# Performance work log

Hardware: AMD Instinct MI355X
Metric: run time of the kernel (lower is better)

The kernel has to match this reference:

```python
import jax, jax.numpy as jnp
import numpy as np

B, Cin, H, W = 8, 256, 32, 32
KS, NH, K = 32, 8, 5          # key_size == value_size, num_heads, kernel_size
STRIDE, PAD = 1, 2
Cout = KS * 3 * NH            # 768
EPS = 1e-5


def setup_inputs() -> dict:
    key = jax.random.key(0)
    k0, k1, k2 = jax.random.split(key, 3)
    return {
        "x": jax.random.normal(k0, (B, Cin, H, W), jnp.float32),
        "conv_w": jax.random.normal(k1, (Cout, Cin), jnp.float32) / np.sqrt(Cin).astype(np.float32),
        "conv_b": jax.random.normal(k2, (Cout,), jnp.float32) * 0.02,
        "gn_w": jnp.ones((Cout,), jnp.float32),
        "gn_b": jnp.zeros((Cout,), jnp.float32),
    }


def reference(x, conv_w, conv_b, gn_w, gn_b):
    Bb = x.shape[0]
    OH = (H + 2 * PAD - K) // STRIDE + 1
    OW = (W + 2 * PAD - K) // STRIDE + 1

    # 1x1 conv: (B, Cout, H, W)
    attn = jnp.einsum('bchw,oc->bohw', x, conv_w) + conv_b[None, :, None, None]

    # unfold / Tile2d -> (B, KH, KW, Cout, OH, OW)
    ap = jnp.pad(attn, ((0, 0), (0, 0), (PAD, PAD), (PAD, PAD)))
    rows = []
    for kh in range(K):
        cols = [ap[:, :, kh:kh + OH * STRIDE:STRIDE, kw:kw + OW * STRIDE:STRIDE]
                for kw in range(K)]
        rows.append(jnp.stack(cols, axis=1))          # (B, KW, C, OH, OW)
    tiles = jnp.stack(rows, axis=1)                   # (B, KH, KW, C, OH, OW)

    # GroupNorm over (group_channels, OH, OW) per (b, kh, kw) sample.
    # groups = 3*NH, group size = KS (each head's key/query/value chunk).
    G = 3 * NH
    t = tiles.reshape(Bb, K, K, G, KS, OH, OW)
    mean = t.mean(axis=(4, 5, 6), keepdims=True)
    var = t.var(axis=(4, 5, 6), keepdims=True)        # biased, like torch GroupNorm
    t = (t - mean) * jax.lax.rsqrt(var + EPS)
    t = t.reshape(Bb, K, K, Cout, OH, OW)
    t = t * gn_w[None, None, None, :, None, None] + gn_b[None, None, None, :, None, None]

    # (B, OH, OW, NH, 3*KS, KH*KW)
    t = t.transpose(0, 4, 5, 3, 1, 2).reshape(Bb, OH, OW, NH, 3 * KS, K * K)
    keyt = t[..., :KS, :]            # (B, OH, OW, NH, KS, KK)
    qt = t[..., KS:2 * KS, :]
    vt = t[..., 2 * KS:, :]          # (B, OH, OW, NH, VS, KK)

    q = qt.mean(axis=-1)             # mean query over the window: (B, OH, OW, NH, KS)
    sal = jnp.einsum('bijnk,bijnkp->bijnp', q, keyt) / np.float32(np.sqrt(KS))
    mask = jax.nn.softmax(sal, axis=-1)               # (B, OH, OW, NH, KK)
    out = jnp.einsum('bijnvp,bijnp->bijnv', vt, mask)  # (B, OH, OW, NH, VS)

    out = out.transpose(0, 3, 4, 1, 2).reshape(Bb, NH * KS, OH, OW)
    return out
```

## Files before the change

kernel.cpp:

```cpp
#include <hip/hip_runtime.h>
#include <hip/hip_bf16.h>

#define B_    8
#define CIN   256
#define COUT  768
#define G_    24
#define PW    40
#define PLANE 1440
#define EPS_  1e-5f

typedef float f32x4 __attribute__((ext_vector_type(4)));
typedef short s16x8 __attribute__((ext_vector_type(8)));
typedef unsigned short ushort_t;
typedef unsigned short u16x4 __attribute__((ext_vector_type(4)));
typedef unsigned long long ull_t;

#define LDS_FENCE() do { asm volatile("" ::: "memory"); \
                         __builtin_amdgcn_s_waitcnt(0xC07F); \
                         asm volatile("" ::: "memory"); } while (0)

static __device__ __forceinline__ ushort_t f2bf(float f) {
    union { float f; unsigned u; } a; a.f = f;
    const unsigned u = a.u;
    const unsigned r = u + 0x7FFFu + ((u >> 16) & 1u);
    return (ushort_t)(r >> 16);
}
static __device__ __forceinline__ float bf2f(ushort_t h) {
    union { unsigned u; float f; } a; a.u = ((unsigned)h) << 16; return a.f;
}
static __device__ __forceinline__ void st4(float* dst, u16x4 v) {
    *(f32x4*)dst = f32x4{ bf2f(v[0]), bf2f(v[1]), bf2f(v[2]), bf2f(v[3]) };
}
static __device__ __forceinline__ unsigned pk2(float lo, float hi) {
    return (unsigned)f2bf(lo) | ((unsigned)f2bf(hi) << 16);
}

__launch_bounds__(256)
__global__ void prep(const float* __restrict__ x, const float* __restrict__ wsrc,
                     ushort_t* __restrict__ xT, ushort_t* __restrict__ wbf) {
    const int bid = blockIdx.x;
    const int t = threadIdx.x;
    if (bid < 512) {
        const int nt = bid & 15, kt = (bid >> 4) & 3, b = bid >> 6;
        const int n0 = nt * 64, k0 = kt * 64;
        __shared__ float Ts[64][65];
        const int kr = t >> 2, c4 = t & 3;
        const float* src = x + (size_t)b * (CIN * 1024) + (size_t)(k0 + kr) * 1024 + n0 + c4 * 16;
        const float4 v0 = *(const float4*)(src + 0);
        const float4 v1 = *(const float4*)(src + 4);
        const float4 v2 = *(const float4*)(src + 8);
        const float4 v3 = *(const float4*)(src + 12);
        float* d = &Ts[kr][c4 * 16];
        *(float4*)(d + 0) = v0; *(float4*)(d + 4) = v1;
        *(float4*)(d + 8) = v2; *(float4*)(d + 12) = v3;
        __syncthreads();
        const int nr = t >> 2, k4 = t & 3;
        unsigned pk[8];
        #pragma unroll
        for (int i = 0; i < 8; ++i)
            pk[i] = pk2(Ts[k4 * 16 + 2 * i][nr], Ts[k4 * 16 + 2 * i + 1][nr]);
        ushort_t* dst = xT + (size_t)b * (1024 * 256) + (size_t)(n0 + nr) * 256 + k0 + k4 * 16;
        *(uint4*)(dst + 0) = uint4{ pk[0], pk[1], pk[2], pk[3] };
        *(uint4*)(dst + 8) = uint4{ pk[4], pk[5], pk[6], pk[7] };
    } else {
        const int wid = bid - 512;
        const size_t idx = (size_t)wid * 2048 + (size_t)t * 8;
        const float4 u0 = *(const float4*)(wsrc + idx);
        const float4 u1 = *(const float4*)(wsrc + idx + 4);
        uint4 o;
        o.x = pk2(u0.x, u0.y); o.y = pk2(u0.z, u0.w);
        o.z = pk2(u1.x, u1.y); o.w = pk2(u1.z, u1.w);
        *(uint4*)(wbf + idx) = o;
    }
}

__launch_bounds__(256)
__global__ void conv_gemm(const ushort_t* __restrict__ wbf, const ushort_t* __restrict__ xT,
                          const float* __restrict__ bias, ushort_t* __restrict__ attn,
                          float* __restrict__ rowAgg) {
    const int t = threadIdx.x;
    const int wv = t >> 6, lane = t & 63;
    const int q = lane >> 4, l15 = lane & 15;
    const int m0 = blockIdx.y * 64;
    const int mw = wv * 16;
    const int n_t = blockIdx.x * 64;
    const int b = n_t >> 10, nl0 = n_t & 1023;
    const int y0 = nl0 >> 5;

    __shared__ ushort_t Bs[64][264];
    ushort_t (*Ct)[2][44] = (ushort_t (*)[2][44])(&Bs[0][0]);
    float (*red)[11]      = (float (*)[11])((char*)(&Bs[0][0]) + 64 * 2 * 44 * 2);

    {
        const ushort_t* src = xT + (size_t)b * (1024 * 256) + (size_t)nl0 * 256;
        #pragma unroll
        for (int i = 0; i < 8; ++i) {
            const int id = i * 256 + t;
            const int row = id >> 5, seg = id & 31;
            *(s16x8*)&Bs[row][seg * 8] = *(const s16x8*)(src + row * 256 + seg * 8);
        }
    }
    __syncthreads();

    const ushort_t* aPf = wbf + (size_t)(m0 + mw + l15) * 256 + q * 8;

    f32x4 acc[4] = {{0,0,0,0},{0,0,0,0},{0,0,0,0},{0,0,0,0}};
    #pragma unroll
    for (int k0 = 0; k0 < 256; k0 += 32) {
        const s16x8 a = *(const s16x8*)(aPf + k0);
        const int kk = k0 + q * 8;
        const s16x8 b0 = *(const s16x8*)&Bs[l15 +  0][kk];
        const s16x8 b1 = *(const s16x8*)&Bs[l15 + 16][kk];
        const s16x8 b2 = *(const s16x8*)&Bs[l15 + 32][kk];
        const s16x8 b3 = *(const s16x8*)&Bs[l15 + 48][kk];
        acc[0] = __builtin_amdgcn_mfma_f32_16x16x32_bf16(a, b0, acc[0], 0, 0, 0);
        acc[1] = __builtin_amdgcn_mfma_f32_16x16x32_bf16(a, b1, acc[1], 0, 0, 0);
        acc[2] = __builtin_amdgcn_mfma_f32_16x16x32_bf16(a, b2, acc[2], 0, 0, 0);
        acc[3] = __builtin_amdgcn_mfma_f32_16x16x32_bf16(a, b3, acc[3], 0, 0, 0);
    }
    __syncthreads();

    float bb[4];
    #pragma unroll
    for (int r = 0; r < 4; ++r) bb[r] = bias[m0 + mw + q * 4 + r];
    #pragma unroll
    for (int j = 0; j < 4; ++j) {
        const int yy = j >> 1, xx = (j & 1) * 16 + l15;
        #pragma unroll
        for (int r = 0; r < 4; ++r)
            Ct[mw + q * 4 + r][yy][2 + xx] = f2bf(acc[j][r] + bb[r]);
    }
    #pragma unroll
    for (int it = 0; it < 2; ++it) {
        const int id = it * 256 + t;
        const int m = id >> 3, yy = (id >> 2) & 1, pos = id & 3;
        const int us = (pos == 0) ? 0 : (32 + 2 * pos);
        *(unsigned*)&Ct[m][yy][us] = 0u;
    }
    __syncthreads();

    ushort_t* pb = attn + ((size_t)(b * COUT + m0)) * PLANE;
    #pragma unroll
    for (int it = 0; it < 5; ++it) {
        const int id = it * 256 + t;
        const int m = id / 20, rem = id % 20, yy = rem / 10, s = rem % 10;
        const ull_t v = *(const ull_t*)&Ct[m][yy][s * 4];
        *(ull_t*)(pb + (size_t)m * PLANE + (y0 + yy + 2) * PW + s * 4) = v;
    }
    if (y0 == 0 || y0 == 30) {
        const int rowA = (y0 == 0) ? 0 : 34;
        #pragma unroll
        for (int it = 0; it < 5; ++it) {
            const int id = it * 256 + t;
            const int m = id / 20, rem = id % 20, yy = rem / 10, s = rem % 10;
            *(ull_t*)(pb + (size_t)m * PLANE + (rowA + yy) * PW + s * 4) = 0ull;
        }
    }

    if (t < 128) {
        const int gi = t >> 6, yy = (t >> 5) & 1, c = t & 31;
        const int m = gi * 32 + c;
        float lin = 0.f, sq = 0.f, e0 = 0.f, e1 = 0.f, e30 = 0.f, e31 = 0.f;
        #pragma unroll
        for (int u = 0; u < 9; ++u) {
            const ull_t vv = *(const ull_t*)&Ct[m][yy][u * 4];
            const unsigned lo = (unsigned)vv, hi = (unsigned)(vv >> 32);
            union { unsigned u; float f; } f0, f1, f2, f3;
            f0.u = lo << 16; f1.u = lo & 0xffff0000u;
            f2.u = hi << 16; f3.u = hi & 0xffff0000u;
            lin += (f0.f + f1.f) + (f2.f + f3.f);
            sq  += (f0.f * f0.f + f1.f * f1.f) + (f2.f * f2.f + f3.f * f3.f);
            if (u == 0) { e0 = f2.f; e1 = f3.f; }
            if (u == 8) { e30 = f0.f; e31 = f1.f; }
        }
        red[t][0] = lin; red[t][1] = sq;
        red[t][2] = e0;  red[t][3] = e0 * e0;
        red[t][4] = e1;  red[t][5] = e1 * e1;
        red[t][6] = e30; red[t][7] = e30 * e30;
        red[t][8] = e31; red[t][9] = e31 * e31;
    }
    __syncthreads();
    if (t < 40) {
        const int s = t % 10, gy = t / 10;
        const int gi = gy >> 1, yy = gy & 1;
        float sum = 0.f;
        #pragma unroll
        for (int c = 0; c < 32; ++c) sum += red[gi * 64 + yy * 32 + c][s];
        const int g = blockIdx.y * 2 + gi;
        rowAgg[(((size_t)b * G_ + g) * 32 + (y0 + yy)) * 10 + s] = sum;
    }
}

__launch_bounds__(128)
__global__ void local_attn(const ushort_t* __restrict__ attn,
                           const float* __restrict__ rowAgg,
                           const float* __restrict__ gn_w, const float* __restrict__ gn_b,
                           float* __restrict__ out) {
    const int wid = blockIdx.x;
    const int b = wid >> 7;
    const int n = (wid >> 4) & 7;
    const int i0 = (wid & 15) * 2;
    const int t = threadIdx.x;
    const int h = t >> 6;
    const int lane = t & 63;
    const int r = lane >> 5;
    const int j = lane & 31;

    __shared__ float KB[2][2][240];
    __shared__ float QB[2][2][240];
    __shared__ float ex[128][27];
    __shared__ float rpL[96][5], rp2L[96][5];
    __shared__ float s_m[75], s_r[75];
    __shared__ float s_rq[25], s_mq[25], s_rk[25], s_ck[25], s_rv[25], s_cv[25];
    __shared__ float s_gw[96], s_gb[96];

    if (t < 96) { s_gw[t] = gn_w[n * 96 + t]; s_gb[t] = gn_b[n * 96 + t]; }

    const float* rab = rowAgg + (size_t)((b * G_ + n * 3) * 32) * 10;
    if (t < 96) {
        const float* a = rab + (size_t)t * 10;
        const float S = a[0], Sq = a[1];
        const float e0 = a[2], q0 = a[3], e1 = a[4], q1 = a[5];
        const float e30 = a[6], q30 = a[7], e31 = a[8], q31 = a[9];
        rpL[t][0] = S - e30 - e31; rpL[t][1] = S - e31; rpL[t][2] = S;
        rpL[t][3] = S - e0;        rpL[t][4] = S - e0 - e1;
        rp2L[t][0] = Sq - q30 - q31; rp2L[t][1] = Sq - q31; rp2L[t][2] = Sq;
        rp2L[t][3] = Sq - q0;        rp2L[t][4] = Sq - q0 - q1;
    }
    __syncthreads();

    if (t < 75) {
        const int gi = t / 25, p = t % 25;
        const int kw = p % 5, kh = p / 5;
        const int rb = gi * 32;
        float cs = 0.f, cs2 = 0.f;
        #pragma unroll
        for (int yy = 0; yy < 32; ++yy) { cs += rpL[rb + yy][kw]; cs2 += rp2L[rb + yy][kw]; }
        if (kh == 0)      { cs -= rpL[rb + 30][kw] + rpL[rb + 31][kw]; cs2 -= rp2L[rb + 30][kw] + rp2L[rb + 31][kw]; }
        else if (kh == 1) { cs -= rpL[rb + 31][kw];                    cs2 -= rp2L[rb + 31][kw]; }
        else if (kh == 3) { cs -= rpL[rb + 0][kw];                     cs2 -= rp2L[rb + 0][kw]; }
        else if (kh == 4) { cs -= rpL[rb + 0][kw] + rpL[rb + 1][kw];   cs2 -= rp2L[rb + 0][kw] + rp2L[rb + 1][kw]; }
        const float inv_n = 1.f / 32768.f;
        const float mean = cs * inv_n;
        const float var  = cs2 * inv_n - mean * mean;
        s_m[t] = mean;
        s_r[t] = rsqrtf(var + EPS_);
    }
    __syncthreads();

    if (t < 25) {
        const float mK = s_m[t],      rK = s_r[t];
        const float mQ = s_m[25 + t], rQ = s_r[25 + t];
        const float mV = s_m[50 + t], rV = s_r[50 + t];
        s_rk[t] = rK; s_ck[t] = mK * rK;
        s_rq[t] = rQ; s_mq[t] = mQ * rQ;
        s_rv[t] = rV; s_cv[t] = mV * rV;
    }
    __syncthreads();

    float rq[25]; float cQ = 0.f;
    #pragma unroll
    for (int p = 0; p < 25; ++p) { rq[p] = s_rq[p]; cQ += s_mq[p]; }

    const ushort_t* regB = attn + (size_t)(b * COUT + n * 96) * PLANE + i0 * PW;
    const bool stg = (lane < 60);
    const int eo = lane * 4;
    const int base = r * PW + j;

    const ushort_t* baseK = regB + (size_t)(h * 16) * PLANE;
    const ushort_t* baseQ = regB + (size_t)(32 + h * 16) * PLANE;
    const ushort_t* baseV = regB + (size_t)(64 + h * 16) * PLANE;

    u16x4 nK{0,0,0,0}, nQ{0,0,0,0}, fK{0,0,0,0}, fQ{0,0,0,0};
    if (stg) {
        const u16x4 c0K = *(const u16x4*)(baseK + eo);
        const u16x4 c0Q = *(const u16x4*)(baseQ + eo);
        st4(&KB[h][0][eo], c0K);
        st4(&QB[h][0][eo], c0Q);
        nK = *(const u16x4*)(baseK + (size_t)PLANE + eo);
        nQ = *(const u16x4*)(baseQ + (size_t)PLANE + eo);
        fK = *(const u16x4*)(baseK + 2 * (size_t)PLANE + eo);
        fQ = *(const u16x4*)(baseQ + 2 * (size_t)PLANE + eo);
    }
    LDS_FENCE();

    float sal[25];
    #pragma unroll
    for (int p = 0; p < 25; ++p) sal[p] = 0.f;
    float sumQ2 = 0.f, sumQB = 0.f;

    for (int cc = 0; cc < 16; ++cc) {
        const int buf = cc & 1;
        if (stg && cc < 15) {
            st4(&KB[h][buf ^ 1][eo], nK);
            st4(&QB[h][buf ^ 1][eo], nQ);
            nK = fK; nQ = fQ;
            if (cc < 13) {
                fK = *(const u16x4*)(baseK + (size_t)(cc + 3) * PLANE + eo);
                fQ = *(const u16x4*)(baseQ + (size_t)(cc + 3) * PLANE + eo);
            } else if (cc == 13) {
                fK = *(const u16x4*)(baseV + eo);
                fQ = *(const u16x4*)(baseV + (size_t)PLANE + eo);
            }
        }
        const int ch = h * 16 + cc;
        const float* qb = &QB[h][buf][base];
        const float* kb = &KB[h][buf][base];
        float qa0 = 0.f, qa1 = 0.f, qa2 = 0.f, qa3 = 0.f, qa4 = 0.f;
        #pragma unroll
        for (int kw = 0; kw < 5; ++kw) {
            qa0 += rq[0 * 5 + kw] * qb[0 * PW + kw];
            qa1 += rq[1 * 5 + kw] * qb[1 * PW + kw];
            qa2 += rq[2 * 5 + kw] * qb[2 * PW + kw];
            qa3 += rq[3 * 5 + kw] * qb[3 * PW + kw];
            qa4 += rq[4 * 5 + kw] * qb[4 * PW + kw];
        }
        const float qa = (qa0 + qa1) + (qa2 + qa3) + qa4;
        const float qk  = s_gw[32 + ch] * ((qa - cQ) * 0.04f) + s_gb[32 + ch];
        const float qk2 = qk * s_gw[ch];
        sumQ2 += qk2; sumQB += qk * s_gb[ch];
        #pragma unroll
        for (int kh = 0; kh < 5; ++kh)
            #pragma unroll
            for (int kw = 0; kw < 5; ++kw)
                sal[kh * 5 + kw] += qk2 * kb[kh * PW + kw];
        LDS_FENCE();
    }

    #pragma unroll
    for (int p = 0; p < 25; ++p) ex[t][p] = sal[p];
    ex[t][25] = sumQ2; ex[t][26] = sumQB;
    if (stg) st4(&KB[h][0][eo], nK);
    __syncthreads();
    const int par = t ^ 64;
    #pragma unroll
    for (int p = 0; p < 25; ++p) sal[p] += ex[par][p];
    sumQ2 += ex[par][25]; sumQB += ex[par][26];

    u16x4 vA = nQ, vB{0,0,0,0};
    if (stg) vB = *(const u16x4*)(baseV + 2 * (size_t)PLANE + eo);

    #pragma unroll
    for (int p = 0; p < 25; ++p) sal[p] = s_rk[p] * sal[p] - s_ck[p] * sumQ2 + sumQB;

    const float scale = 0.17677669529663687f;
    float mmax = -3.4e38f;
    #pragma unroll
    for (int p = 0; p < 25; ++p) { sal[p] *= scale; mmax = fmaxf(mmax, sal[p]); }
    float ssum = 0.f;
    #pragma unroll
    for (int p = 0; p < 25; ++p) { sal[p] = __expf(sal[p] - mmax); ssum += sal[p]; }
    const float rs = 1.f / ssum;
    float cV2 = 0.f;
    #pragma unroll
    for (int p = 0; p < 25; ++p) {
        const float m = sal[p] * rs;
        sal[p] = m * s_rv[p];
        cV2 += m * s_cv[p];
    }
    LDS_FENCE();

    for (int cc = 0; cc < 16; ++cc) {
        const int buf = cc & 1;
        if (stg && cc < 15) {
            st4(&KB[h][buf ^ 1][eo], vA);
            vA = vB;
            if (cc < 13) vB = *(const u16x4*)(baseV + (size_t)(cc + 3) * PLANE + eo);
        }
        const int v = h * 16 + cc;
        const float* vb = &KB[h][buf][base];
        float a0 = 0.f, a1 = 0.f, a2 = 0.f, a3 = 0.f, a4 = 0.f;
        #pragma unroll
        for (int kw = 0; kw < 5; ++kw) {
            a0 += sal[0 * 5 + kw] * vb[0 * PW + kw];
            a1 += sal[1 * 5 + kw] * vb[1 * PW + kw];
            a2 += sal[2 * 5 + kw] * vb[2 * PW + kw];
            a3 += sal[3 * 5 + kw] * vb[3 * PW + kw];
            a4 += sal[4 * 5 + kw] * vb[4 * PW + kw];
        }
        const float acc = (a0 + a1) + (a2 + a3) + a4;
        out[((size_t)(b * 256 + n * 32 + v) * 32 + (i0 + r)) * 32 + j] =
            s_gw[64 + v] * acc + (s_gb[64 + v] - s_gw[64 + v] * cV2);
        LDS_FENCE();
    }
}

extern "C" void kernel_launch(void* const* d_in, const int* in_sizes, int n_in,
                              void* d_out, int out_size, void* d_ws, size_t ws_size,
                              hipStream_t stream) {
    const float* x      = (const float*)d_in[0];
    const float* conv_w = (const float*)d_in[1];
    const float* conv_b = (const float*)d_in[2];
    const float* gn_w   = (const float*)d_in[3];
    const float* gn_b   = (const float*)d_in[4];
    float* out = (float*)d_out;

    ushort_t* attn    = (ushort_t*)d_ws;
    float*    rowAgg  = (float*)(attn + 8847360);
    ushort_t* xT      = (ushort_t*)(rowAgg + 61440);
    ushort_t* wbf     = xT + 2097152;

    prep<<<608, 256, 0, stream>>>(x, conv_w, xT, wbf);
    conv_gemm<<<dim3(128, 12), 256, 0, stream>>>(wbf, xT, conv_b, attn, rowAgg);
    local_attn<<<1024, 128, 0, stream>>>(attn, rowAgg, gn_w, gn_b, out);
}
```

Measured before the change: 110.2 us.

## Deepen register prefetch pipeline and swizzle block order across XCDs

Global loads of K/Q/V planes are now prefetched four channels ahead through a rotating set of eight register vectors instead of two ahead. The V prefetch is chained from the tail of the K/Q loop so loads for the value phase are in flight early. Both channel loops are fully unrolled. Block indices are remapped so each group of blocks sharing a batch lands on the same XCD, which should improve L2 reuse. The costs are higher register pressure, larger code size, and fiddly index bookkeeping in the rotating buffers.

```diff
diff --git a/kernel.cpp b/kernel.cpp
--- a/kernel.cpp
+++ b/kernel.cpp
@@ -196,7 +196,8 @@
                            const float* __restrict__ rowAgg,
                            const float* __restrict__ gn_w, const float* __restrict__ gn_b,
                            float* __restrict__ out) {
-    const int wid = blockIdx.x;
+    const int bx = blockIdx.x;
+    const int wid = (bx & 7) * 128 + (bx >> 3);
     const int b = wid >> 7;
     const int n = (wid >> 4) & 7;
     const int i0 = (wid & 15) * 2;
@@ -271,16 +272,21 @@
     const ushort_t* baseQ = regB + (size_t)(32 + h * 16) * PLANE;
     const ushort_t* baseV = regB + (size_t)(64 + h * 16) * PLANE;
 
-    u16x4 nK{0,0,0,0}, nQ{0,0,0,0}, fK{0,0,0,0}, fQ{0,0,0,0};
+    u16x4 k1{0,0,0,0}, k2{0,0,0,0}, k3{0,0,0,0}, k4{0,0,0,0};
+    u16x4 q1{0,0,0,0}, q2{0,0,0,0}, q3{0,0,0,0}, q4{0,0,0,0};
     if (stg) {
         const u16x4 c0K = *(const u16x4*)(baseK + eo);
         const u16x4 c0Q = *(const u16x4*)(baseQ + eo);
         st4(&KB[h][0][eo], c0K);
         st4(&QB[h][0][eo], c0Q);
-        nK = *(const u16x4*)(baseK + (size_t)PLANE + eo);
-        nQ = *(const u16x4*)(baseQ + (size_t)PLANE + eo);
-        fK = *(const u16x4*)(baseK + 2 * (size_t)PLANE + eo);
-        fQ = *(const u16x4*)(baseQ + 2 * (size_t)PLANE + eo);
+        k1 = *(const u16x4*)(baseK + 1 * (size_t)PLANE + eo);
+        q1 = *(const u16x4*)(baseQ + 1 * (size_t)PLANE + eo);
+        k2 = *(const u16x4*)(baseK + 2 * (size_t)PLANE + eo);
+        q2 = *(const u16x4*)(baseQ + 2 * (size_t)PLANE + eo);
+        k3 = *(const u16x4*)(baseK + 3 * (size_t)PLANE + eo);
+        q3 = *(const u16x4*)(baseQ + 3 * (size_t)PLANE + eo);
+        k4 = *(const u16x4*)(baseK + 4 * (size_t)PLANE + eo);
+        q4 = *(const u16x4*)(baseQ + 4 * (size_t)PLANE + eo);
     }
     LDS_FENCE();
 
@@ -289,18 +295,20 @@
     for (int p = 0; p < 25; ++p) sal[p] = 0.f;
     float sumQ2 = 0.f, sumQB = 0.f;
 
+    #pragma unroll
     for (int cc = 0; cc < 16; ++cc) {
         const int buf = cc & 1;
         if (stg && cc < 15) {
-            st4(&KB[h][buf ^ 1][eo], nK);
-            st4(&QB[h][buf ^ 1][eo], nQ);
-            nK = fK; nQ = fQ;
-            if (cc < 13) {
-                fK = *(const u16x4*)(baseK + (size_t)(cc + 3) * PLANE + eo);
-                fQ = *(const u16x4*)(baseQ + (size_t)(cc + 3) * PLANE + eo);
-            } else if (cc == 13) {
-                fK = *(const u16x4*)(baseV + eo);
-                fQ = *(const u16x4*)(baseV + (size_t)PLANE + eo);
+            st4(&KB[h][buf ^ 1][eo], k1);
+            st4(&QB[h][buf ^ 1][eo], q1);
+            k1 = k2; k2 = k3; k3 = k4;
+            q1 = q2; q2 = q3; q3 = q4;
+            if (cc < 11) {
+                k4 = *(const u16x4*)(baseK + (size_t)(cc + 5) * PLANE + eo);
+                q4 = *(const u16x4*)(baseQ + (size_t)(cc + 5) * PLANE + eo);
+            } else {
+                k4 = *(const u16x4*)(baseV + (size_t)(cc - 11) * PLANE + eo);
+                q4 = *(const u16x4*)(baseV + (size_t)(cc - 7) * PLANE + eo);
             }
         }
         const int ch = h * 16 + cc;
@@ -330,15 +338,12 @@
     #pragma unroll
     for (int p = 0; p < 25; ++p) ex[t][p] = sal[p];
     ex[t][25] = sumQ2; ex[t][26] = sumQB;
-    if (stg) st4(&KB[h][0][eo], nK);
+    if (stg) st4(&KB[h][0][eo], k1);
     __syncthreads();
     const int par = t ^ 64;
     #pragma unroll
     for (int p = 0; p < 25; ++p) sal[p] += ex[par][p];
     sumQ2 += ex[par][25]; sumQB += ex[par][26];
-
-    u16x4 vA = nQ, vB{0,0,0,0};
-    if (stg) vB = *(const u16x4*)(baseV + 2 * (size_t)PLANE + eo);
 
     #pragma unroll
     for (int p = 0; p < 25; ++p) sal[p] = s_rk[p] * sal[p] - s_ck[p] * sumQ2 + sumQB;
@@ -360,12 +365,14 @@
     }
     LDS_FENCE();
 
+    #pragma unroll
     for (int cc = 0; cc < 16; ++cc) {
         const int buf = cc & 1;
         if (stg && cc < 15) {
-            st4(&KB[h][buf ^ 1][eo], vA);
-            vA = vB;
-            if (cc < 13) vB = *(const u16x4*)(baseV + (size_t)(cc + 3) * PLANE + eo);
+            st4(&KB[h][buf ^ 1][eo], k2);
+            k2 = k3; k3 = k4; k4 = q1; q1 = q2; q2 = q3; q3 = q4;
+            if (cc < 8)
+                q4 = *(const u16x4*)(baseV + (size_t)(cc + 8) * PLANE + eo);
         }
         const int v = h * 16 + cc;
         const float* vb = &KB[h][buf][base];
```

Measured after the change: 202.6 us. 1.84x slower.

## Double conv GEMM M-tile to reuse shared B tile; remap local_attn block order

Applied to the files above, without the earlier changes.

The conv GEMM block now covers 128 output channels instead of 64, and each wave computes two 16-row MFMA tiles against the same shared-memory B fragments. This halves the number of blocks that stage the same x tile into LDS. The epilogue, padding, store loops and group-stat reduction are widened to match. Separately, local_attn permutes its block index so that consecutive blocks interleave batches and heads, which is meant to improve cache locality or load spread. The trade-offs are more accumulator registers, fewer blocks (768) for the GPU's CUs, and a larger Ct/red region in the reused LDS buffer.

```diff
diff --git a/kernel.cpp b/kernel.cpp
--- a/kernel.cpp
+++ b/kernel.cpp
@@ -81,15 +81,15 @@
     const int t = threadIdx.x;
     const int wv = t >> 6, lane = t & 63;
     const int q = lane >> 4, l15 = lane & 15;
-    const int m0 = blockIdx.y * 64;
-    const int mw = wv * 16;
+    const int m0 = blockIdx.y * 128;
+    const int mw = wv * 32;
     const int n_t = blockIdx.x * 64;
     const int b = n_t >> 10, nl0 = n_t & 1023;
     const int y0 = nl0 >> 5;
 
     __shared__ ushort_t Bs[64][264];
     ushort_t (*Ct)[2][44] = (ushort_t (*)[2][44])(&Bs[0][0]);
-    float (*red)[11]      = (float (*)[11])((char*)(&Bs[0][0]) + 64 * 2 * 44 * 2);
+    float (*red)[11]      = (float (*)[11])((char*)(&Bs[0][0]) + 128 * 2 * 44 * 2);
 
     {
         const ushort_t* src = xT + (size_t)b * (1024 * 256) + (size_t)nl0 * 256;
@@ -102,36 +102,48 @@
     }
     __syncthreads();
 
-    const ushort_t* aPf = wbf + (size_t)(m0 + mw + l15) * 256 + q * 8;
-
-    f32x4 acc[4] = {{0,0,0,0},{0,0,0,0},{0,0,0,0},{0,0,0,0}};
+    const ushort_t* aPf0 = wbf + (size_t)(m0 + mw + l15) * 256 + q * 8;
+    const ushort_t* aPf1 = aPf0 + 16 * 256;
+
+    f32x4 acc0[4] = {{0,0,0,0},{0,0,0,0},{0,0,0,0},{0,0,0,0}};
+    f32x4 acc1[4] = {{0,0,0,0},{0,0,0,0},{0,0,0,0},{0,0,0,0}};
     #pragma unroll
     for (int k0 = 0; k0 < 256; k0 += 32) {
-        const s16x8 a = *(const s16x8*)(aPf + k0);
+        const s16x8 a0 = *(const s16x8*)(aPf0 + k0);
+        const s16x8 a1 = *(const s16x8*)(aPf1 + k0);
         const int kk = k0 + q * 8;
         const s16x8 b0 = *(const s16x8*)&Bs[l15 +  0][kk];
         const s16x8 b1 = *(const s16x8*)&Bs[l15 + 16][kk];
         const s16x8 b2 = *(const s16x8*)&Bs[l15 + 32][kk];
         const s16x8 b3 = *(const s16x8*)&Bs[l15 + 48][kk];
-        acc[0] = __builtin_amdgcn_mfma_f32_16x16x32_bf16(a, b0, acc[0], 0, 0, 0);
-        acc[1] = __builtin_amdgcn_mfma_f32_16x16x32_bf16(a, b1, acc[1], 0, 0, 0);
-        acc[2] = __builtin_amdgcn_mfma_f32_16x16x32_bf16(a, b2, acc[2], 0, 0, 0);
-        acc[3] = __builtin_amdgcn_mfma_f32_16x16x32_bf16(a, b3, acc[3], 0, 0, 0);
-    }
-    __syncthreads();
-
-    float bb[4];
-    #pragma unroll
-    for (int r = 0; r < 4; ++r) bb[r] = bias[m0 + mw + q * 4 + r];
+        acc0[0] = __builtin_amdgcn_mfma_f32_16x16x32_bf16(a0, b0, acc0[0], 0, 0, 0);
+        acc0[1] = __builtin_amdgcn_mfma_f32_16x16x32_bf16(a0, b1, acc0[1], 0, 0, 0);
+        acc0[2] = __builtin_amdgcn_mfma_f32_16x16x32_bf16(a0, b2, acc0[2], 0, 0, 0);
+        acc0[3] = __builtin_amdgcn_mfma_f32_16x16x32_bf16(a0, b3, acc0[3], 0, 0, 0);
+        acc1[0] = __builtin_amdgcn_mfma_f32_16x16x32_bf16(a1, b0, acc1[0], 0, 0, 0);
+        acc1[1] = __builtin_amdgcn_mfma_f32_16x16x32_bf16(a1, b1, acc1[1], 0, 0, 0);
+        acc1[2] = __builtin_amdgcn_mfma_f32_16x16x32_bf16(a1, b2, acc1[2], 0, 0, 0);
+        acc1[3] = __builtin_amdgcn_mfma_f32_16x16x32_bf16(a1, b3, acc1[3], 0, 0, 0);
+    }
+    __syncthreads();
+
+    float bb0[4], bb1[4];
+    #pragma unroll
+    for (int r = 0; r < 4; ++r) {
+        bb0[r] = bias[m0 + mw + q * 4 + r];
+        bb1[r] = bias[m0 + mw + 16 + q * 4 + r];
+    }
     #pragma unroll
     for (int j = 0; j < 4; ++j) {
         const int yy = j >> 1, xx = (j & 1) * 16 + l15;
         #pragma unroll
-        for (int r = 0; r < 4; ++r)
-            Ct[mw + q * 4 + r][yy][2 + xx] = f2bf(acc[j][r] + bb[r]);
-    }
-    #pragma unroll
-    for (int it = 0; it < 2; ++it) {
+        for (int r = 0; r < 4; ++r) {
+            Ct[mw + q * 4 + r][yy][2 + xx]      = f2bf(acc0[j][r] + bb0[r]);
+            Ct[mw + 16 + q * 4 + r][yy][2 + xx] = f2bf(acc1[j][r] + bb1[r]);
+        }
+    }
+    #pragma unroll
+    for (int it = 0; it < 4; ++it) {
         const int id = it * 256 + t;
         const int m = id >> 3, yy = (id >> 2) & 1, pos = id & 3;
         const int us = (pos == 0) ? 0 : (32 + 2 * pos);
@@ -141,7 +153,7 @@
 
     ushort_t* pb = attn + ((size_t)(b * COUT + m0)) * PLANE;
     #pragma unroll
-    for (int it = 0; it < 5; ++it) {
+    for (int it = 0; it < 10; ++it) {
         const int id = it * 256 + t;
         const int m = id / 20, rem = id % 20, yy = rem / 10, s = rem % 10;
         const ull_t v = *(const ull_t*)&Ct[m][yy][s * 4];
@@ -150,14 +162,14 @@
     if (y0 == 0 || y0 == 30) {
         const int rowA = (y0 == 0) ? 0 : 34;
         #pragma unroll
-        for (int it = 0; it < 5; ++it) {
+        for (int it = 0; it < 10; ++it) {
             const int id = it * 256 + t;
             const int m = id / 20, rem = id % 20, yy = rem / 10, s = rem % 10;
             *(ull_t*)(pb + (size_t)m * PLANE + (rowA + yy) * PW + s * 4) = 0ull;
         }
     }
 
-    if (t < 128) {
+    {
         const int gi = t >> 6, yy = (t >> 5) & 1, c = t & 31;
         const int m = gi * 32 + c;
         float lin = 0.f, sq = 0.f, e0 = 0.f, e1 = 0.f, e30 = 0.f, e31 = 0.f;
@@ -180,13 +192,13 @@
         red[t][8] = e31; red[t][9] = e31 * e31;
     }
     __syncthreads();
-    if (t < 40) {
+    if (t < 80) {
         const int s = t % 10, gy = t / 10;
         const int gi = gy >> 1, yy = gy & 1;
         float sum = 0.f;
         #pragma unroll
         for (int c = 0; c < 32; ++c) sum += red[gi * 64 + yy * 32 + c][s];
-        const int g = blockIdx.y * 2 + gi;
+        const int g = blockIdx.y * 4 + gi;
         rowAgg[(((size_t)b * G_ + g) * 32 + (y0 + yy)) * 10 + s] = sum;
     }
 }
@@ -196,7 +208,8 @@
                            const float* __restrict__ rowAgg,
                            const float* __restrict__ gn_w, const float* __restrict__ gn_b,
                            float* __restrict__ out) {
-    const int wid = blockIdx.x;
+    const int bx = blockIdx.x;
+    const int wid = (bx & 7) * 128 + (bx >> 3);
     const int b = wid >> 7;
     const int n = (wid >> 4) & 7;
     const int i0 = (wid & 15) * 2;
@@ -401,6 +414,6 @@
     ushort_t* wbf     = xT + 2097152;
 
     prep<<<608, 256, 0, stream>>>(x, conv_w, xT, wbf);
-    conv_gemm<<<dim3(128, 12), 256, 0, stream>>>(wbf, xT, conv_b, attn, rowAgg);
+    conv_gemm<<<dim3(128, 6), 256, 0, stream>>>(wbf, xT, conv_b, attn, rowAgg);
     local_attn<<<1024, 128, 0, stream>>>(attn, rowAgg, gn_w, gn_b, out);
 }
```

Result: slower. 113.8 us (+3.2%).
